# Performance work log

Hardware: AMD Instinct MI355X
Metric: run time of the kernel (lower is better)

## Reference

```python
import jax, jax.numpy as jnp
import numpy as np

N, X_DIM, Y_DIM, HID = 1024, 256, 256, 256  # HID = hidden_size // 2


def setup_inputs() -> dict:
    key = jax.random.key(0)
    ks = jax.random.split(key, 11)
    s_in = 1.0 / np.sqrt(X_DIM)
    s_h = 1.0 / np.sqrt(HID)
    return {
        "x_samples": jax.random.normal(ks[0], (N, X_DIM), jnp.float32),
        "y_samples": jax.random.normal(ks[1], (N, Y_DIM), jnp.float32),
        "z_samples": jax.random.normal(ks[2], (N, Y_DIM), jnp.float32),
        "w1_mu": jax.random.uniform(ks[3], (HID, X_DIM), jnp.float32, -s_in, s_in),
        "b1_mu": jax.random.uniform(ks[4], (HID,), jnp.float32, -s_in, s_in),
        "w2_mu": jax.random.uniform(ks[5], (Y_DIM, HID), jnp.float32, -s_h, s_h),
        "b2_mu": jax.random.uniform(ks[6], (Y_DIM,), jnp.float32, -s_h, s_h),
        "w1_lv": jax.random.uniform(ks[7], (HID, X_DIM), jnp.float32, -s_in, s_in),
        "b1_lv": jax.random.uniform(ks[8], (HID,), jnp.float32, -s_in, s_in),
        "w2_lv": jax.random.uniform(ks[9], (Y_DIM, HID), jnp.float32, -s_h, s_h),
        "b2_lv": jax.random.uniform(ks[10], (Y_DIM,), jnp.float32, -s_h, s_h),
    }


def reference(x_samples, y_samples, z_samples,
              w1_mu, b1_mu, w2_mu, b2_mu,
              w1_lv, b1_lv, w2_lv, b2_lv):
    # MLP heads (torch Linear: x @ W.T + b)
    h_mu = jax.nn.relu(x_samples @ w1_mu.T + b1_mu)
    mu = h_mu @ w2_mu.T + b2_mu                       # [N, D]
    h_lv = jax.nn.relu(x_samples @ w1_lv.T + b1_lv)
    logvar = jnp.tanh(h_lv @ w2_lv.T + b2_lv)          # [N, D]

    inv2var = 1.0 / (2.0 * jnp.exp(logvar))           # [N, D]

    # positive: per-sample conditional log-density term
    positive = -((mu - y_samples) ** 2 + (mu - z_samples) ** 2) * inv2var  # [N, D]

    # negative: mean over all pairings (i: prediction, j: sample)
    # pairwise squared diffs materialize [N, N, D] like the original broadcast
    pred = mu[:, None, :]                              # [N, 1, D]
    sq = (y_samples[None, :, :] - pred) ** 2 + (z_samples[None, :, :] - pred) ** 2
    negative = -sq.mean(axis=1) * inv2var              # [N, D]

    return jax.nn.relu(positive.sum(axis=-1) - negative.sum(axis=-1)).mean()
```

## Files before the change

kernel.cpp:

```cpp
#include <hip/hip_runtime.h>
#include <math.h>

constexpr int LSB = 72;

typedef short bf16x8 __attribute__((ext_vector_type(8)));
typedef float f32x4  __attribute__((ext_vector_type(4)));

__device__ __forceinline__ unsigned short f2bf_rne(float f) {
    unsigned u = __float_as_uint(f);
    unsigned r = (u + 0x7fff + ((u >> 16) & 1)) >> 16;
    return (unsigned short)r;
}
__device__ __forceinline__ float bf2f(unsigned short h) {
    return __uint_as_float(((unsigned)h) << 16);
}
__device__ __forceinline__ void split4(float4 v, ushort4& hi, ushort4& lo) {
    hi.x = f2bf_rne(v.x); lo.x = f2bf_rne(v.x - bf2f(hi.x));
    hi.y = f2bf_rne(v.y); lo.y = f2bf_rne(v.y - bf2f(hi.y));
    hi.z = f2bf_rne(v.z); lo.z = f2bf_rne(v.z - bf2f(hi.z));
    hi.w = f2bf_rne(v.w); lo.w = f2bf_rne(v.w - bf2f(hi.w));
}

__global__ __launch_bounds__(256, 2)
void k1_layer1(const float* __restrict__ x,
               const float* __restrict__ w1m, const float* __restrict__ w1l,
               const float* __restrict__ b1m, const float* __restrict__ b1l,
               const float* __restrict__ w2m, const float* __restrict__ w2l,
               unsigned short* __restrict__ hmH, unsigned short* __restrict__ hmL,
               unsigned short* __restrict__ hlH, unsigned short* __restrict__ hlL,
               unsigned short* __restrict__ w2mH, unsigned short* __restrict__ w2mL,
               unsigned short* __restrict__ w2lH, unsigned short* __restrict__ w2lL,
               const float* __restrict__ y, const float* __restrict__ z,
               float* __restrict__ pA1, float* __restrict__ pB1,
               float* __restrict__ rowAcc) {
    const int bid = blockIdx.x, t = threadIdx.x;

    if (bid >= 512) {
        int m = bid - 512;
        float sA = 0.f, sB = 0.f;
        int base = m * 64 * 256 + t;
        for (int j = 0; j < 64; j++) {
            float yv = y[base + j * 256];
            float zv = z[base + j * 256];
            sA += yv * yv + zv * zv;
            sB += yv + zv;
        }
        pA1[m * 256 + t] = sA;
        pB1[m * 256 + t] = sB;
        return;
    }

    const int head = bid & 1, ct = (bid >> 1) & 7, rt = bid >> 4;
    const int rowBase = rt * 32, colBase = ct * 32;
    const int w = t >> 6, lane = t & 63, quad = lane >> 4, mr = lane & 15;
    const int mt = w & 1, nt = w >> 1;

    const float* Bw   = head ? w1l : w1m;
    const float* bias = head ? b1l : b1m;
    unsigned short* CH = head ? hlH : hmH;
    unsigned short* CL = head ? hlL : hmL;

    __shared__ __align__(16) unsigned short Ah[32][LSB], Al[32][LSB];
    __shared__ __align__(16) unsigned short Bh[32][LSB], Bl[32][LSB];

    f32x4 acc = {0.f, 0.f, 0.f, 0.f};

    for (int kt = 0; kt < 256; kt += 64) {
#pragma unroll
        for (int p = 0; p < 2; p++) {
            int idx = p * 256 + t;
            int r = idx >> 4, k4 = idx & 15;
            float4 av = *(const float4*)&x[(rowBase + r) * 256 + kt + k4 * 4];
            float4 bv = *(const float4*)&Bw[(colBase + r) * 256 + kt + k4 * 4];
            ushort4 h4, l4;
            split4(av, h4, l4);
            *(ushort4*)&Ah[r][k4 * 4] = h4;
            *(ushort4*)&Al[r][k4 * 4] = l4;
            split4(bv, h4, l4);
            *(ushort4*)&Bh[r][k4 * 4] = h4;
            *(ushort4*)&Bl[r][k4 * 4] = l4;
        }
        __syncthreads();

#pragma unroll
        for (int kk = 0; kk < 64; kk += 32) {
            int ko = kk + quad * 8;
            bf16x8 ah = *(const bf16x8*)&Ah[mt * 16 + mr][ko];
            bf16x8 al = *(const bf16x8*)&Al[mt * 16 + mr][ko];
            bf16x8 bh = *(const bf16x8*)&Bh[nt * 16 + mr][ko];
            bf16x8 bl = *(const bf16x8*)&Bl[nt * 16 + mr][ko];
            acc = __builtin_amdgcn_mfma_f32_16x16x32_bf16(ah, bh, acc, 0, 0, 0);
            acc = __builtin_amdgcn_mfma_f32_16x16x32_bf16(ah, bl, acc, 0, 0, 0);
            acc = __builtin_amdgcn_mfma_f32_16x16x32_bf16(al, bh, acc, 0, 0, 0);
        }
        __syncthreads();
    }

    {
        int cg = colBase + nt * 16 + mr;
        float bb = bias[cg];
#pragma unroll
        for (int reg = 0; reg < 4; reg++) {
            int rg = rowBase + mt * 16 + quad * 4 + reg;
            float v = fmaxf(acc[reg] + bb, 0.f);
            unsigned short hi = f2bf_rne(v);
            CH[rg * 256 + cg] = hi;
            CL[rg * 256 + cg] = f2bf_rne(v - bf2f(hi));
        }
    }

    if (bid < 256) {
        int off = bid * 256 + t;
        float vm = w2m[off], vl = w2l[off];
        unsigned short h1 = f2bf_rne(vm);
        w2mH[off] = h1; w2mL[off] = f2bf_rne(vm - bf2f(h1));
        unsigned short h2 = f2bf_rne(vl);
        w2lH[off] = h2; w2lL[off] = f2bf_rne(vl - bf2f(h2));
    }

    if (bid < 4) rowAcc[bid * 256 + t] = 0.f;
}

__global__ __launch_bounds__(256, 2)
void k2_fused(const unsigned short* __restrict__ hmH, const unsigned short* __restrict__ hmL,
              const unsigned short* __restrict__ hlH, const unsigned short* __restrict__ hlL,
              const unsigned short* __restrict__ w2mH, const unsigned short* __restrict__ w2mL,
              const unsigned short* __restrict__ w2lH, const unsigned short* __restrict__ w2lL,
              const float* __restrict__ b2m, const float* __restrict__ b2l,
              const float* __restrict__ y, const float* __restrict__ z,
              const float* __restrict__ pA1, const float* __restrict__ pB1,
              float* __restrict__ rowAcc) {
    const int bid = blockIdx.x, t = threadIdx.x;
    const int rt = bid >> 4, ct = bid & 15;
    const int rowBase = rt * 32, colBase = ct * 16;
    const int w = t >> 6, lane = t & 63, quad = lane >> 4, mr = lane & 15;
    const int h = w & 1, mt = w >> 1;

    __shared__ __align__(16) unsigned short Ast[2][2][32][LSB];
    __shared__ __align__(16) unsigned short Bst[2][2][16][LSB];
    __shared__ float Cx[2][32][17];
    __shared__ float partA[16][16], partB[16][16];
    __shared__ float mAf[16], mBf[16];

    const unsigned short* Aarr[4] = {hmH, hmL, hlH, hlL};
    const unsigned short* Barr[4] = {w2mH, w2mL, w2lH, w2lL};

    {
        int s = t >> 4, c = t & 15;
        partA[s][c] = pA1[s * 256 + colBase + c];
        partB[s][c] = pB1[s * 256 + colBase + c];
    }
    __syncthreads();
    if (t < 16) {
        float sA = 0.f, sB = 0.f;
#pragma unroll
        for (int s = 0; s < 16; s++) { sA += partA[s][t]; sB += partB[s][t]; }
        mAf[t] = sA * (1.f / 1024.f);
        mBf[t] = sB * (1.f / 1024.f);
    }

    f32x4 acc = {0.f, 0.f, 0.f, 0.f};

    for (int kt = 0; kt < 256; kt += 64) {
#pragma unroll
        for (int hp = 0; hp < 4; hp++) {
#pragma unroll
            for (int p = 0; p < 2; p++) {
                int idx = p * 256 + t;
                int r = idx >> 4, k4 = idx & 15;
                *(ushort4*)&Ast[hp >> 1][hp & 1][r][k4 * 4] =
                    *(const ushort4*)&Aarr[hp][(rowBase + r) * 256 + kt + k4 * 4];
            }
            {
                int r = t >> 4, k4 = t & 15;
                *(ushort4*)&Bst[hp >> 1][hp & 1][r][k4 * 4] =
                    *(const ushort4*)&Barr[hp][(colBase + r) * 256 + kt + k4 * 4];
            }
        }
        __syncthreads();

#pragma unroll
        for (int kk = 0; kk < 64; kk += 32) {
            int ko = kk + quad * 8;
            bf16x8 ah = *(const bf16x8*)&Ast[h][0][mt * 16 + mr][ko];
            bf16x8 al = *(const bf16x8*)&Ast[h][1][mt * 16 + mr][ko];
            bf16x8 bh = *(const bf16x8*)&Bst[h][0][mr][ko];
            bf16x8 bl = *(const bf16x8*)&Bst[h][1][mr][ko];
            acc = __builtin_amdgcn_mfma_f32_16x16x32_bf16(ah, bh, acc, 0, 0, 0);
            acc = __builtin_amdgcn_mfma_f32_16x16x32_bf16(ah, bl, acc, 0, 0, 0);
            acc = __builtin_amdgcn_mfma_f32_16x16x32_bf16(al, bh, acc, 0, 0, 0);
        }
        __syncthreads();
    }

    {
        const float* bias = h ? b2l : b2m;
        float bb = bias[colBase + mr];
#pragma unroll
        for (int reg = 0; reg < 4; reg++)
            Cx[h][mt * 16 + quad * 4 + reg][mr] = acc[reg] + bb;
    }
    __syncthreads();

    {
        int col = t & 15, rg = t >> 4;
        int gcol = colBase + col;
        float mA = mAf[col], mB = mBf[col];
#pragma unroll
        for (int rr = 0; rr < 2; rr++) {
            int row = rg * 2 + rr;
            int o = (rowBase + row) * 256 + gcol;
            float m  = Cx[0][row][col];
            float lv = tanhf(Cx[1][row][col]);
            float iv = 0.5f * expf(-lv);
            float yv = y[o];
            float zv = z[o];
            float Mt = mA - 2.f * m * mB + 2.f * m * m;
            float dy = m - yv, dz = m - zv;
            float term = iv * (Mt - dy * dy - dz * dz);
#pragma unroll
            for (int msk = 8; msk; msk >>= 1)
                term += __shfl_xor(term, msk, 16);
            if (col == 0) atomicAdd(&rowAcc[rowBase + row], term);
        }
    }
}

__global__ __launch_bounds__(256)
void k3_final(const float* __restrict__ rowAcc, float* __restrict__ out) {
    __shared__ float red[4];
    int t = threadIdx.x, lane = t & 63, wave = t >> 6;
    float v = 0.f;
#pragma unroll
    for (int p = 0; p < 4; p++)
        v += fmaxf(rowAcc[p * 256 + t], 0.f);
#pragma unroll
    for (int msk = 32; msk; msk >>= 1)
        v += __shfl_xor(v, msk, 64);
    if (lane == 0) red[wave] = v;
    __syncthreads();
    if (t == 0)
        out[0] = (red[0] + red[1] + red[2] + red[3]) * (1.f / 1024.f);
}

extern "C" void kernel_launch(void* const* d_in, const int* in_sizes, int n_in,
                              void* d_out, int out_size, void* d_ws, size_t ws_size,
                              hipStream_t stream) {
    const float* x   = (const float*)d_in[0];
    const float* y   = (const float*)d_in[1];
    const float* zs  = (const float*)d_in[2];
    const float* w1m = (const float*)d_in[3];
    const float* b1m = (const float*)d_in[4];
    const float* w2m = (const float*)d_in[5];
    const float* b2m = (const float*)d_in[6];
    const float* w1l = (const float*)d_in[7];
    const float* b1l = (const float*)d_in[8];
    const float* w2l = (const float*)d_in[9];
    const float* b2l = (const float*)d_in[10];
    float* out = (float*)d_out;

    char* ws = (char*)d_ws;
    float* pA1    = (float*)(ws);
    float* pB1    = (float*)(ws + (256u << 10));
    float* rowAcc = (float*)(ws + (512u << 10));
    unsigned short* hmH = (unsigned short*)(ws + (1024u << 10));
    unsigned short* hmL = (unsigned short*)(ws + (1536u << 10));
    unsigned short* hlH = (unsigned short*)(ws + (2048u << 10));
    unsigned short* hlL = (unsigned short*)(ws + (2560u << 10));
    unsigned short* w2mH = (unsigned short*)(ws + (3072u << 10));
    unsigned short* w2mL = (unsigned short*)(ws + (3200u << 10));
    unsigned short* w2lH = (unsigned short*)(ws + (3328u << 10));
    unsigned short* w2lL = (unsigned short*)(ws + (3456u << 10));

    k1_layer1<<<528, 256, 0, stream>>>(x, w1m, w1l, b1m, b1l, w2m, w2l,
                                       hmH, hmL, hlH, hlL,
                                       w2mH, w2mL, w2lH, w2lL,
                                       y, zs, pA1, pB1, rowAcc);
    k2_fused<<<512, 256, 0, stream>>>(hmH, hmL, hlH, hlL,
                                      w2mH, w2mL, w2lH, w2lL,
                                      b2m, b2l, y, zs, pA1, pB1, rowAcc);
    k3_final<<<1, 256, 0, stream>>>(rowAcc, out);
}
```

Baseline: 92.14 us.

## Fuse both MLP layers and loss into one row-block kernel with double-buffered weights

Splits all weights into bf16 hi/lo in a small prep kernel, which also computes the column sums of y and z and zeroes the output. A single fused kernel then processes 16 rows per block. It keeps the hidden activations in shared memory, streams W1 and W2 tiles through a register-prefetched double buffer, and reduces the loss per row before one atomic per block. This removes the global round trip of the hidden activations and two kernel launches. In exchange it launches only 64 blocks, so most compute units sit idle and each block streams the full weight set serially.

```diff
diff --git a/kernel.cpp b/kernel.cpp
--- a/kernel.cpp
+++ b/kernel.cpp
@@ -21,22 +21,51 @@
     hi.w = f2bf_rne(v.w); lo.w = f2bf_rne(v.w - bf2f(hi.w));
 }
 
-__global__ __launch_bounds__(256, 2)
-void k1_layer1(const float* __restrict__ x,
-               const float* __restrict__ w1m, const float* __restrict__ w1l,
-               const float* __restrict__ b1m, const float* __restrict__ b1l,
-               const float* __restrict__ w2m, const float* __restrict__ w2l,
-               unsigned short* __restrict__ hmH, unsigned short* __restrict__ hmL,
-               unsigned short* __restrict__ hlH, unsigned short* __restrict__ hlL,
-               unsigned short* __restrict__ w2mH, unsigned short* __restrict__ w2mL,
-               unsigned short* __restrict__ w2lH, unsigned short* __restrict__ w2lL,
-               const float* __restrict__ y, const float* __restrict__ z,
-               float* __restrict__ pA1, float* __restrict__ pB1,
-               float* __restrict__ rowAcc) {
+struct Pre { bf16x8 v0, v1, v2, v3; };
+
+__device__ __forceinline__ void stage_load(Pre& p,
+        const unsigned short* __restrict__ H0, const unsigned short* __restrict__ L0,
+        const unsigned short* __restrict__ H1, const unsigned short* __restrict__ L1,
+        int colB, int kB, int t) {
+    int off = (colB + (t >> 3)) * 256 + kB + (t & 7) * 8;
+    p.v0 = *(const bf16x8*)&H0[off];
+    p.v1 = *(const bf16x8*)&L0[off];
+    p.v2 = *(const bf16x8*)&H1[off];
+    p.v3 = *(const bf16x8*)&L1[off];
+}
+__device__ __forceinline__ void stage_write(const Pre& p, unsigned short* b, int t) {
+    unsigned short* d = b + (t >> 3) * LSB + (t & 7) * 8;
+    *(bf16x8*)(d        ) = p.v0;
+    *(bf16x8*)(d +  4608) = p.v1;
+    *(bf16x8*)(d +  9216) = p.v2;
+    *(bf16x8*)(d + 13824) = p.v3;
+}
+
+__global__ __launch_bounds__(256)
+void k0_prep(const float* __restrict__ w1m, const float* __restrict__ w1l,
+             const float* __restrict__ w2m, const float* __restrict__ w2l,
+             const float* __restrict__ y, const float* __restrict__ z,
+             unsigned short* __restrict__ w1mH, unsigned short* __restrict__ w1mL,
+             unsigned short* __restrict__ w1lH, unsigned short* __restrict__ w1lL,
+             unsigned short* __restrict__ w2mH, unsigned short* __restrict__ w2mL,
+             unsigned short* __restrict__ w2lH, unsigned short* __restrict__ w2lL,
+             float* __restrict__ pA1, float* __restrict__ pB1,
+             float* __restrict__ out) {
     const int bid = blockIdx.x, t = threadIdx.x;
-
-    if (bid >= 512) {
-        int m = bid - 512;
+    if (bid < 64) {
+        int off = bid * 1024 + t * 4;
+        float4 v; ushort4 h4, l4;
+        v = *(const float4*)&w1m[off]; split4(v, h4, l4);
+        *(ushort4*)&w1mH[off] = h4; *(ushort4*)&w1mL[off] = l4;
+        v = *(const float4*)&w1l[off]; split4(v, h4, l4);
+        *(ushort4*)&w1lH[off] = h4; *(ushort4*)&w1lL[off] = l4;
+        v = *(const float4*)&w2m[off]; split4(v, h4, l4);
+        *(ushort4*)&w2mH[off] = h4; *(ushort4*)&w2mL[off] = l4;
+        v = *(const float4*)&w2l[off]; split4(v, h4, l4);
+        *(ushort4*)&w2lH[off] = h4; *(ushort4*)&w2lL[off] = l4;
+    } else {
+        int m = bid - 64;
+        if (m == 0 && t == 0) out[0] = 0.f;
         float sA = 0.f, sB = 0.f;
         int base = m * 64 * 256 + t;
         for (int j = 0; j < 64; j++) {
@@ -47,200 +76,152 @@
         }
         pA1[m * 256 + t] = sA;
         pB1[m * 256 + t] = sB;
-        return;
-    }
-
-    const int head = bid & 1, ct = (bid >> 1) & 7, rt = bid >> 4;
-    const int rowBase = rt * 32, colBase = ct * 32;
-    const int w = t >> 6, lane = t & 63, quad = lane >> 4, mr = lane & 15;
-    const int mt = w & 1, nt = w >> 1;
-
-    const float* Bw   = head ? w1l : w1m;
-    const float* bias = head ? b1l : b1m;
-    unsigned short* CH = head ? hlH : hmH;
-    unsigned short* CL = head ? hlL : hmL;
-
-    __shared__ __align__(16) unsigned short Ah[32][LSB], Al[32][LSB];
-    __shared__ __align__(16) unsigned short Bh[32][LSB], Bl[32][LSB];
-
-    f32x4 acc = {0.f, 0.f, 0.f, 0.f};
-
-    for (int kt = 0; kt < 256; kt += 64) {
-#pragma unroll
-        for (int p = 0; p < 2; p++) {
-            int idx = p * 256 + t;
-            int r = idx >> 4, k4 = idx & 15;
-            float4 av = *(const float4*)&x[(rowBase + r) * 256 + kt + k4 * 4];
-            float4 bv = *(const float4*)&Bw[(colBase + r) * 256 + kt + k4 * 4];
-            ushort4 h4, l4;
-            split4(av, h4, l4);
-            *(ushort4*)&Ah[r][k4 * 4] = h4;
-            *(ushort4*)&Al[r][k4 * 4] = l4;
-            split4(bv, h4, l4);
-            *(ushort4*)&Bh[r][k4 * 4] = h4;
-            *(ushort4*)&Bl[r][k4 * 4] = l4;
-        }
-        __syncthreads();
-
-#pragma unroll
-        for (int kk = 0; kk < 64; kk += 32) {
-            int ko = kk + quad * 8;
-            bf16x8 ah = *(const bf16x8*)&Ah[mt * 16 + mr][ko];
-            bf16x8 al = *(const bf16x8*)&Al[mt * 16 + mr][ko];
-            bf16x8 bh = *(const bf16x8*)&Bh[nt * 16 + mr][ko];
-            bf16x8 bl = *(const bf16x8*)&Bl[nt * 16 + mr][ko];
-            acc = __builtin_amdgcn_mfma_f32_16x16x32_bf16(ah, bh, acc, 0, 0, 0);
-            acc = __builtin_amdgcn_mfma_f32_16x16x32_bf16(ah, bl, acc, 0, 0, 0);
-            acc = __builtin_amdgcn_mfma_f32_16x16x32_bf16(al, bh, acc, 0, 0, 0);
-        }
-        __syncthreads();
-    }
-
-    {
-        int cg = colBase + nt * 16 + mr;
-        float bb = bias[cg];
+    }
+}
+
+__global__ __launch_bounds__(512)
+void kf_fused(const float* __restrict__ x, const float* __restrict__ y, const float* __restrict__ z,
+              const float* __restrict__ b1m, const float* __restrict__ b1l,
+              const float* __restrict__ b2m, const float* __restrict__ b2l,
+              const unsigned short* __restrict__ w1mH, const unsigned short* __restrict__ w1mL,
+              const unsigned short* __restrict__ w1lH, const unsigned short* __restrict__ w1lL,
+              const unsigned short* __restrict__ w2mH, const unsigned short* __restrict__ w2mL,
+              const unsigned short* __restrict__ w2lH, const unsigned short* __restrict__ w2lL,
+              const float* __restrict__ pA1, const float* __restrict__ pB1,
+              float* __restrict__ out) {
+    const int bid = blockIdx.x, t = threadIdx.x;
+    const int R0 = bid << 4;
+    const int lane = t & 63, quad = lane >> 4, mr = lane & 15;
+    const int wv = t >> 6, h = wv & 1, nt = wv >> 1;
+
+    __shared__ __align__(16) unsigned short Ax[2][16][264];
+    __shared__ __align__(16) unsigned short Hb[2][2][16][264];
+    __shared__ __align__(16) unsigned short BtF[2][18432];
+    __shared__ float Cx[2][16][68];
+    __shared__ float mAf[256], mBf[256], rowSum[16];
+
+    if (t < 256) {
+        float sA = 0.f, sB = 0.f;
+#pragma unroll
+        for (int sI = 0; sI < 16; sI++) { sA += pA1[sI * 256 + t]; sB += pB1[sI * 256 + t]; }
+        mAf[t] = sA * (1.f / 1024.f);
+        mBf[t] = sB * (1.f / 1024.f);
+    }
+    if (t < 16) rowSum[t] = 0.f;
+#pragma unroll
+    for (int p = 0; p < 2; p++) {
+        int idx = p * 512 + t;
+        int r = idx >> 6, k4 = idx & 63;
+        float4 av = *(const float4*)&x[(R0 + r) * 256 + k4 * 4];
+        ushort4 h4, l4; split4(av, h4, l4);
+        *(ushort4*)&Ax[0][r][k4 * 4] = h4;
+        *(ushort4*)&Ax[1][r][k4 * 4] = l4;
+    }
+
+    Pre pre;
+    stage_load(pre, w1mH, w1mL, w1lH, w1lL, 0, 0, t);
+
+    int s = 0;
+    for (int cg = 0; cg < 4; cg++) {
+        f32x4 acc = {0.f, 0.f, 0.f, 0.f};
+        for (int kt = 0; kt < 4; kt++, s++) {
+            unsigned short* b = BtF[s & 1];
+            stage_write(pre, b, t);
+            if (s < 15) stage_load(pre, w1mH, w1mL, w1lH, w1lL,
+                                   ((s + 1) >> 2) << 6, ((s + 1) & 3) << 6, t);
+            else        stage_load(pre, w2mH, w2mL, w2lH, w2lL, 0, 0, t);
+            __syncthreads();
+            const unsigned short* bHp = b + (h * 2 + 0) * 4608 + (nt * 16 + mr) * LSB;
+            const unsigned short* bLp = b + (h * 2 + 1) * 4608 + (nt * 16 + mr) * LSB;
+            const unsigned short* aHp = &Ax[0][mr][kt * 64];
+            const unsigned short* aLp = &Ax[1][mr][kt * 64];
+#pragma unroll
+            for (int ks = 0; ks < 2; ks++) {
+                int ko = ks * 32 + quad * 8;
+                bf16x8 ah = *(const bf16x8*)&aHp[ko];
+                bf16x8 al = *(const bf16x8*)&aLp[ko];
+                bf16x8 bh = *(const bf16x8*)&bHp[ko];
+                bf16x8 bl = *(const bf16x8*)&bLp[ko];
+                acc = __builtin_amdgcn_mfma_f32_16x16x32_bf16(ah, bh, acc, 0, 0, 0);
+                acc = __builtin_amdgcn_mfma_f32_16x16x32_bf16(ah, bl, acc, 0, 0, 0);
+                acc = __builtin_amdgcn_mfma_f32_16x16x32_bf16(al, bh, acc, 0, 0, 0);
+            }
+        }
+        int gcol = cg * 64 + nt * 16 + mr;
+        float bb = (h ? b1l : b1m)[gcol];
 #pragma unroll
         for (int reg = 0; reg < 4; reg++) {
-            int rg = rowBase + mt * 16 + quad * 4 + reg;
             float v = fmaxf(acc[reg] + bb, 0.f);
             unsigned short hi = f2bf_rne(v);
-            CH[rg * 256 + cg] = hi;
-            CL[rg * 256 + cg] = f2bf_rne(v - bf2f(hi));
-        }
-    }
-
-    if (bid < 256) {
-        int off = bid * 256 + t;
-        float vm = w2m[off], vl = w2l[off];
-        unsigned short h1 = f2bf_rne(vm);
-        w2mH[off] = h1; w2mL[off] = f2bf_rne(vm - bf2f(h1));
-        unsigned short h2 = f2bf_rne(vl);
-        w2lH[off] = h2; w2lL[off] = f2bf_rne(vl - bf2f(h2));
-    }
-
-    if (bid < 4) rowAcc[bid * 256 + t] = 0.f;
-}
-
-__global__ __launch_bounds__(256, 2)
-void k2_fused(const unsigned short* __restrict__ hmH, const unsigned short* __restrict__ hmL,
-              const unsigned short* __restrict__ hlH, const unsigned short* __restrict__ hlL,
-              const unsigned short* __restrict__ w2mH, const unsigned short* __restrict__ w2mL,
-              const unsigned short* __restrict__ w2lH, const unsigned short* __restrict__ w2lL,
-              const float* __restrict__ b2m, const float* __restrict__ b2l,
-              const float* __restrict__ y, const float* __restrict__ z,
-              const float* __restrict__ pA1, const float* __restrict__ pB1,
-              float* __restrict__ rowAcc) {
-    const int bid = blockIdx.x, t = threadIdx.x;
-    const int rt = bid >> 4, ct = bid & 15;
-    const int rowBase = rt * 32, colBase = ct * 16;
-    const int w = t >> 6, lane = t & 63, quad = lane >> 4, mr = lane & 15;
-    const int h = w & 1, mt = w >> 1;
-
-    __shared__ __align__(16) unsigned short Ast[2][2][32][LSB];
-    __shared__ __align__(16) unsigned short Bst[2][2][16][LSB];
-    __shared__ float Cx[2][32][17];
-    __shared__ float partA[16][16], partB[16][16];
-    __shared__ float mAf[16], mBf[16];
-
-    const unsigned short* Aarr[4] = {hmH, hmL, hlH, hlL};
-    const unsigned short* Barr[4] = {w2mH, w2mL, w2lH, w2lL};
-
-    {
-        int s = t >> 4, c = t & 15;
-        partA[s][c] = pA1[s * 256 + colBase + c];
-        partB[s][c] = pB1[s * 256 + colBase + c];
-    }
-    __syncthreads();
+            Hb[h][0][quad * 4 + reg][gcol] = hi;
+            Hb[h][1][quad * 4 + reg][gcol] = f2bf_rne(v - bf2f(hi));
+        }
+    }
+
+    for (int cg = 0; cg < 4; cg++) {
+        f32x4 acc = {0.f, 0.f, 0.f, 0.f};
+        for (int kt = 0; kt < 4; kt++, s++) {
+            unsigned short* b = BtF[s & 1];
+            stage_write(pre, b, t);
+            if (s < 31) {
+                int nn = s - 15;
+                stage_load(pre, w2mH, w2mL, w2lH, w2lL, (nn >> 2) << 6, (nn & 3) << 6, t);
+            }
+            __syncthreads();
+            const unsigned short* bHp = b + (h * 2 + 0) * 4608 + (nt * 16 + mr) * LSB;
+            const unsigned short* bLp = b + (h * 2 + 1) * 4608 + (nt * 16 + mr) * LSB;
+            const unsigned short* aHp = &Hb[h][0][mr][kt * 64];
+            const unsigned short* aLp = &Hb[h][1][mr][kt * 64];
+#pragma unroll
+            for (int ks = 0; ks < 2; ks++) {
+                int ko = ks * 32 + quad * 8;
+                bf16x8 ah = *(const bf16x8*)&aHp[ko];
+                bf16x8 al = *(const bf16x8*)&aLp[ko];
+                bf16x8 bh = *(const bf16x8*)&bHp[ko];
+                bf16x8 bl = *(const bf16x8*)&bLp[ko];
+                acc = __builtin_amdgcn_mfma_f32_16x16x32_bf16(ah, bh, acc, 0, 0, 0);
+                acc = __builtin_amdgcn_mfma_f32_16x16x32_bf16(ah, bl, acc, 0, 0, 0);
+                acc = __builtin_amdgcn_mfma_f32_16x16x32_bf16(al, bh, acc, 0, 0, 0);
+            }
+        }
+        {
+            float bb = (h ? b2l : b2m)[cg * 64 + nt * 16 + mr];
+#pragma unroll
+            for (int reg = 0; reg < 4; reg++)
+                Cx[h][quad * 4 + reg][nt * 16 + mr] = acc[reg] + bb;
+        }
+        __syncthreads();
+        {
+            int r = t >> 5, c0 = t & 31;
+            float v = 0.f;
+#pragma unroll
+            for (int j = 0; j < 2; j++) {
+                int c = c0 + 32 * j;
+                int gcol = cg * 64 + c;
+                float m  = Cx[0][r][c];
+                float lv = tanhf(Cx[1][r][c]);
+                float iv = 0.5f * expf(-lv);
+                int o = (R0 + r) * 256 + gcol;
+                float yv = y[o], zv = z[o];
+                float Mt = mAf[gcol] - 2.f * m * mBf[gcol] + 2.f * m * m;
+                float dy = m - yv, dz = m - zv;
+                v += iv * (Mt - dy * dy - dz * dz);
+            }
+#pragma unroll
+            for (int msk = 16; msk; msk >>= 1)
+                v += __shfl_xor(v, msk, 32);
+            if (c0 == 0) rowSum[r] += v;
+        }
+        __syncthreads();
+    }
+
     if (t < 16) {
-        float sA = 0.f, sB = 0.f;
-#pragma unroll
-        for (int s = 0; s < 16; s++) { sA += partA[s][t]; sB += partB[s][t]; }
-        mAf[t] = sA * (1.f / 1024.f);
-        mBf[t] = sB * (1.f / 1024.f);
-    }
-
-    f32x4 acc = {0.f, 0.f, 0.f, 0.f};
-
-    for (int kt = 0; kt < 256; kt += 64) {
-#pragma unroll
-        for (int hp = 0; hp < 4; hp++) {
-#pragma unroll
-            for (int p = 0; p < 2; p++) {
-                int idx = p * 256 + t;
-                int r = idx >> 4, k4 = idx & 15;
-                *(ushort4*)&Ast[hp >> 1][hp & 1][r][k4 * 4] =
-                    *(const ushort4*)&Aarr[hp][(rowBase + r) * 256 + kt + k4 * 4];
-            }
-            {
-                int r = t >> 4, k4 = t & 15;
-                *(ushort4*)&Bst[hp >> 1][hp & 1][r][k4 * 4] =
-                    *(const ushort4*)&Barr[hp][(colBase + r) * 256 + kt + k4 * 4];
-            }
-        }
-        __syncthreads();
-
-#pragma unroll
-        for (int kk = 0; kk < 64; kk += 32) {
-            int ko = kk + quad * 8;
-            bf16x8 ah = *(const bf16x8*)&Ast[h][0][mt * 16 + mr][ko];
-            bf16x8 al = *(const bf16x8*)&Ast[h][1][mt * 16 + mr][ko];
-            bf16x8 bh = *(const bf16x8*)&Bst[h][0][mr][ko];
-            bf16x8 bl = *(const bf16x8*)&Bst[h][1][mr][ko];
-            acc = __builtin_amdgcn_mfma_f32_16x16x32_bf16(ah, bh, acc, 0, 0, 0);
-            acc = __builtin_amdgcn_mfma_f32_16x16x32_bf16(ah, bl, acc, 0, 0, 0);
-            acc = __builtin_amdgcn_mfma_f32_16x16x32_bf16(al, bh, acc, 0, 0, 0);
-        }
-        __syncthreads();
-    }
-
-    {
-        const float* bias = h ? b2l : b2m;
-        float bb = bias[colBase + mr];
-#pragma unroll
-        for (int reg = 0; reg < 4; reg++)
-            Cx[h][mt * 16 + quad * 4 + reg][mr] = acc[reg] + bb;
-    }
-    __syncthreads();
-
-    {
-        int col = t & 15, rg = t >> 4;
-        int gcol = colBase + col;
-        float mA = mAf[col], mB = mBf[col];
-#pragma unroll
-        for (int rr = 0; rr < 2; rr++) {
-            int row = rg * 2 + rr;
-            int o = (rowBase + row) * 256 + gcol;
-            float m  = Cx[0][row][col];
-            float lv = tanhf(Cx[1][row][col]);
-            float iv = 0.5f * expf(-lv);
-            float yv = y[o];
-            float zv = z[o];
-            float Mt = mA - 2.f * m * mB + 2.f * m * m;
-            float dy = m - yv, dz = m - zv;
-            float term = iv * (Mt - dy * dy - dz * dz);
-#pragma unroll
-            for (int msk = 8; msk; msk >>= 1)
-                term += __shfl_xor(term, msk, 16);
-            if (col == 0) atomicAdd(&rowAcc[rowBase + row], term);
-        }
-    }
-}
-
-__global__ __launch_bounds__(256)
-void k3_final(const float* __restrict__ rowAcc, float* __restrict__ out) {
-    __shared__ float red[4];
-    int t = threadIdx.x, lane = t & 63, wave = t >> 6;
-    float v = 0.f;
-#pragma unroll
-    for (int p = 0; p < 4; p++)
-        v += fmaxf(rowAcc[p * 256 + t], 0.f);
-#pragma unroll
-    for (int msk = 32; msk; msk >>= 1)
-        v += __shfl_xor(v, msk, 64);
-    if (lane == 0) red[wave] = v;
-    __syncthreads();
-    if (t == 0)
-        out[0] = (red[0] + red[1] + red[2] + red[3]) * (1.f / 1024.f);
+        float v = fmaxf(rowSum[t], 0.f);
+#pragma unroll
+        for (int msk = 8; msk; msk >>= 1)
+            v += __shfl_xor(v, msk, 16);
+        if (t == 0) atomicAdd(out, v * (1.f / 1024.f));
+    }
 }
 
 extern "C" void kernel_launch(void* const* d_in, const int* in_sizes, int n_in,
@@ -260,24 +241,23 @@
     float* out = (float*)d_out;
 
     char* ws = (char*)d_ws;
-    float* pA1    = (float*)(ws);
-    float* pB1    = (float*)(ws + (256u << 10));
-    float* rowAcc = (float*)(ws + (512u << 10));
-    unsigned short* hmH = (unsigned short*)(ws + (1024u << 10));
-    unsigned short* hmL = (unsigned short*)(ws + (1536u << 10));
-    unsigned short* hlH = (unsigned short*)(ws + (2048u << 10));
-    unsigned short* hlL = (unsigned short*)(ws + (2560u << 10));
-    unsigned short* w2mH = (unsigned short*)(ws + (3072u << 10));
-    unsigned short* w2mL = (unsigned short*)(ws + (3200u << 10));
-    unsigned short* w2lH = (unsigned short*)(ws + (3328u << 10));
-    unsigned short* w2lL = (unsigned short*)(ws + (3456u << 10));
-
-    k1_layer1<<<528, 256, 0, stream>>>(x, w1m, w1l, b1m, b1l, w2m, w2l,
-                                       hmH, hmL, hlH, hlL,
-                                       w2mH, w2mL, w2lH, w2lL,
-                                       y, zs, pA1, pB1, rowAcc);
-    k2_fused<<<512, 256, 0, stream>>>(hmH, hmL, hlH, hlL,
-                                      w2mH, w2mL, w2lH, w2lL,
-                                      b2m, b2l, y, zs, pA1, pB1, rowAcc);
-    k3_final<<<1, 256, 0, stream>>>(rowAcc, out);
-}
+    float* pA1 = (float*)(ws);
+    float* pB1 = (float*)(ws + (64u  << 10));
+    unsigned short* w1mH = (unsigned short*)(ws + (128u  << 10));
+    unsigned short* w1mL = (unsigned short*)(ws + (256u  << 10));
+    unsigned short* w1lH = (unsigned short*)(ws + (384u  << 10));
+    unsigned short* w1lL = (unsigned short*)(ws + (512u  << 10));
+    unsigned short* w2mH = (unsigned short*)(ws + (640u  << 10));
+    unsigned short* w2mL = (unsigned short*)(ws + (768u  << 10));
+    unsigned short* w2lH = (unsigned short*)(ws + (896u  << 10));
+    unsigned short* w2lL = (unsigned short*)(ws + (1024u << 10));
+
+    k0_prep<<<80, 256, 0, stream>>>(w1m, w1l, w2m, w2l, y, zs,
+                                    w1mH, w1mL, w1lH, w1lL,
+                                    w2mH, w2mL, w2lH, w2lL,
+                                    pA1, pB1, out);
+    kf_fused<<<64, 512, 0, stream>>>(x, y, zs, b1m, b1l, b2m, b2l,
+                                     w1mH, w1mL, w1lH, w1lL,
+                                     w2mH, w2mL, w2lH, w2lL,
+                                     pA1, pB1, out);
+}
```

Result: slower. 98.24 us (+6.6%).

## Load MFMA operands directly from global memory, dropping LDS staging in both GEMMs

Applied to the files above, without the earlier changes.

Both GEMM kernels stop staging tiles in shared memory with __syncthreads and instead have each lane load its MFMA fragments (8 contiguous elements per k-step) straight from global memory. The first kernel converts fp32 to hi/lo bf16 in registers per fragment. This removes LDS traffic and barriers. The cost is redundant global/L2 reads: operands shared across waves are now fetched separately by each wave, and the hi/lo split in the first kernel is recomputed per wave instead of once per tile.

```diff
diff --git a/kernel.cpp b/kernel.cpp
--- a/kernel.cpp
+++ b/kernel.cpp
@@ -1,7 +1,6 @@
 #include <hip/hip_runtime.h>
 #include <math.h>
 
-constexpr int LSB = 72;
 
 typedef short bf16x8 __attribute__((ext_vector_type(8)));
 typedef float f32x4  __attribute__((ext_vector_type(4)));
@@ -19,6 +18,18 @@
     hi.y = f2bf_rne(v.y); lo.y = f2bf_rne(v.y - bf2f(hi.y));
     hi.z = f2bf_rne(v.z); lo.z = f2bf_rne(v.z - bf2f(hi.z));
     hi.w = f2bf_rne(v.w); lo.w = f2bf_rne(v.w - bf2f(hi.w));
+}
+__device__ __forceinline__ void split8(const float* __restrict__ p,
+                                       bf16x8& hi, bf16x8& lo) {
+    float4 v0 = *(const float4*)p;
+    float4 v1 = *(const float4*)(p + 4);
+    float a[8] = {v0.x, v0.y, v0.z, v0.w, v1.x, v1.y, v1.z, v1.w};
+#pragma unroll
+    for (int i = 0; i < 8; i++) {
+        unsigned short h = f2bf_rne(a[i]);
+        hi[i] = (short)h;
+        lo[i] = (short)f2bf_rne(a[i] - bf2f(h));
+    }
 }
 
 __global__ __launch_bounds__(256, 2)
@@ -60,40 +71,19 @@
     unsigned short* CH = head ? hlH : hmH;
     unsigned short* CL = head ? hlL : hmL;
 
-    __shared__ __align__(16) unsigned short Ah[32][LSB], Al[32][LSB];
-    __shared__ __align__(16) unsigned short Bh[32][LSB], Bl[32][LSB];
+    const float* ax = &x [(rowBase + mt * 16 + mr) * 256];
+    const float* bw = &Bw[(colBase + nt * 16 + mr) * 256];
 
     f32x4 acc = {0.f, 0.f, 0.f, 0.f};
-
-    for (int kt = 0; kt < 256; kt += 64) {
-#pragma unroll
-        for (int p = 0; p < 2; p++) {
-            int idx = p * 256 + t;
-            int r = idx >> 4, k4 = idx & 15;
-            float4 av = *(const float4*)&x[(rowBase + r) * 256 + kt + k4 * 4];
-            float4 bv = *(const float4*)&Bw[(colBase + r) * 256 + kt + k4 * 4];
-            ushort4 h4, l4;
-            split4(av, h4, l4);
-            *(ushort4*)&Ah[r][k4 * 4] = h4;
-            *(ushort4*)&Al[r][k4 * 4] = l4;
-            split4(bv, h4, l4);
-            *(ushort4*)&Bh[r][k4 * 4] = h4;
-            *(ushort4*)&Bl[r][k4 * 4] = l4;
-        }
-        __syncthreads();
-
-#pragma unroll
-        for (int kk = 0; kk < 64; kk += 32) {
-            int ko = kk + quad * 8;
-            bf16x8 ah = *(const bf16x8*)&Ah[mt * 16 + mr][ko];
-            bf16x8 al = *(const bf16x8*)&Al[mt * 16 + mr][ko];
-            bf16x8 bh = *(const bf16x8*)&Bh[nt * 16 + mr][ko];
-            bf16x8 bl = *(const bf16x8*)&Bl[nt * 16 + mr][ko];
-            acc = __builtin_amdgcn_mfma_f32_16x16x32_bf16(ah, bh, acc, 0, 0, 0);
-            acc = __builtin_amdgcn_mfma_f32_16x16x32_bf16(ah, bl, acc, 0, 0, 0);
-            acc = __builtin_amdgcn_mfma_f32_16x16x32_bf16(al, bh, acc, 0, 0, 0);
-        }
-        __syncthreads();
+#pragma unroll
+    for (int ks = 0; ks < 8; ks++) {
+        int k0 = ks * 32 + quad * 8;
+        bf16x8 ah, al, bh, bl;
+        split8(&ax[k0], ah, al);
+        split8(&bw[k0], bh, bl);
+        acc = __builtin_amdgcn_mfma_f32_16x16x32_bf16(ah, bh, acc, 0, 0, 0);
+        acc = __builtin_amdgcn_mfma_f32_16x16x32_bf16(ah, bl, acc, 0, 0, 0);
+        acc = __builtin_amdgcn_mfma_f32_16x16x32_bf16(al, bh, acc, 0, 0, 0);
     }
 
     {
@@ -136,15 +126,10 @@
     const int w = t >> 6, lane = t & 63, quad = lane >> 4, mr = lane & 15;
     const int h = w & 1, mt = w >> 1;
 
-    __shared__ __align__(16) unsigned short Ast[2][2][32][LSB];
-    __shared__ __align__(16) unsigned short Bst[2][2][16][LSB];
     __shared__ float Cx[2][32][17];
     __shared__ float partA[16][16], partB[16][16];
     __shared__ float mAf[16], mBf[16];
 
-    const unsigned short* Aarr[4] = {hmH, hmL, hlH, hlL};
-    const unsigned short* Barr[4] = {w2mH, w2mL, w2lH, w2lL};
-
     {
         int s = t >> 4, c = t & 15;
         partA[s][c] = pA1[s * 256 + colBase + c];
@@ -159,38 +144,26 @@
         mBf[t] = sB * (1.f / 1024.f);
     }
 
+    const unsigned short* AH = h ? hlH : hmH;
+    const unsigned short* AL = h ? hlL : hmL;
+    const unsigned short* BH = h ? w2lH : w2mH;
+    const unsigned short* BL = h ? w2lL : w2mL;
+    const unsigned short* aH = &AH[(rowBase + mt * 16 + mr) * 256];
+    const unsigned short* aL = &AL[(rowBase + mt * 16 + mr) * 256];
+    const unsigned short* bH = &BH[(colBase + mr) * 256];
+    const unsigned short* bL = &BL[(colBase + mr) * 256];
+
     f32x4 acc = {0.f, 0.f, 0.f, 0.f};
-
-    for (int kt = 0; kt < 256; kt += 64) {
-#pragma unroll
-        for (int hp = 0; hp < 4; hp++) {
-#pragma unroll
-            for (int p = 0; p < 2; p++) {
-                int idx = p * 256 + t;
-                int r = idx >> 4, k4 = idx & 15;
-                *(ushort4*)&Ast[hp >> 1][hp & 1][r][k4 * 4] =
-                    *(const ushort4*)&Aarr[hp][(rowBase + r) * 256 + kt + k4 * 4];
-            }
-            {
-                int r = t >> 4, k4 = t & 15;
-                *(ushort4*)&Bst[hp >> 1][hp & 1][r][k4 * 4] =
-                    *(const ushort4*)&Barr[hp][(colBase + r) * 256 + kt + k4 * 4];
-            }
-        }
-        __syncthreads();
-
-#pragma unroll
-        for (int kk = 0; kk < 64; kk += 32) {
-            int ko = kk + quad * 8;
-            bf16x8 ah = *(const bf16x8*)&Ast[h][0][mt * 16 + mr][ko];
-            bf16x8 al = *(const bf16x8*)&Ast[h][1][mt * 16 + mr][ko];
-            bf16x8 bh = *(const bf16x8*)&Bst[h][0][mr][ko];
-            bf16x8 bl = *(const bf16x8*)&Bst[h][1][mr][ko];
-            acc = __builtin_amdgcn_mfma_f32_16x16x32_bf16(ah, bh, acc, 0, 0, 0);
-            acc = __builtin_amdgcn_mfma_f32_16x16x32_bf16(ah, bl, acc, 0, 0, 0);
-            acc = __builtin_amdgcn_mfma_f32_16x16x32_bf16(al, bh, acc, 0, 0, 0);
-        }
-        __syncthreads();
+#pragma unroll
+    for (int ks = 0; ks < 8; ks++) {
+        int k0 = ks * 32 + quad * 8;
+        bf16x8 ah = *(const bf16x8*)&aH[k0];
+        bf16x8 al = *(const bf16x8*)&aL[k0];
+        bf16x8 bh = *(const bf16x8*)&bH[k0];
+        bf16x8 bl = *(const bf16x8*)&bL[k0];
+        acc = __builtin_amdgcn_mfma_f32_16x16x32_bf16(ah, bh, acc, 0, 0, 0);
+        acc = __builtin_amdgcn_mfma_f32_16x16x32_bf16(ah, bl, acc, 0, 0, 0);
+        acc = __builtin_amdgcn_mfma_f32_16x16x32_bf16(al, bh, acc, 0, 0, 0);
     }
 
     {
```

Result: slower. 96.98 us (+5.3%).

## Load full-K layer1 tiles once and fold y/z column sums into GEMM blocks

Applied to the files above, without the earlier changes.

Layer-1 GEMM blocks now stage the whole K=256 slice of x and W1 (hi/lo bf16 split) into LDS in one pass, then run all MFMA steps without the per-64-K reload and barrier pairs. The separate 16 reduction blocks for y/z column statistics are removed, and the first 64 GEMM blocks compute 16-row partial sums instead. k2 now sums 64 partials per column instead of 16. The larger LDS footprint (about 67KB per block) may lower occupancy and drops the overlap of loads with MFMA.

```diff
diff --git a/kernel.cpp b/kernel.cpp
--- a/kernel.cpp
+++ b/kernel.cpp
@@ -1,7 +1,7 @@
 #include <hip/hip_runtime.h>
 #include <math.h>
 
-constexpr int LSB = 72;
+constexpr int LSK = 264;
 
 typedef short bf16x8 __attribute__((ext_vector_type(8)));
 typedef float f32x4  __attribute__((ext_vector_type(4)));
@@ -35,21 +35,6 @@
                float* __restrict__ rowAcc) {
     const int bid = blockIdx.x, t = threadIdx.x;
 
-    if (bid >= 512) {
-        int m = bid - 512;
-        float sA = 0.f, sB = 0.f;
-        int base = m * 64 * 256 + t;
-        for (int j = 0; j < 64; j++) {
-            float yv = y[base + j * 256];
-            float zv = z[base + j * 256];
-            sA += yv * yv + zv * zv;
-            sB += yv + zv;
-        }
-        pA1[m * 256 + t] = sA;
-        pB1[m * 256 + t] = sB;
-        return;
-    }
-
     const int head = bid & 1, ct = (bid >> 1) & 7, rt = bid >> 4;
     const int rowBase = rt * 32, colBase = ct * 32;
     const int w = t >> 6, lane = t & 63, quad = lane >> 4, mr = lane & 15;
@@ -60,40 +45,41 @@
     unsigned short* CH = head ? hlH : hmH;
     unsigned short* CL = head ? hlL : hmL;
 
-    __shared__ __align__(16) unsigned short Ah[32][LSB], Al[32][LSB];
-    __shared__ __align__(16) unsigned short Bh[32][LSB], Bl[32][LSB];
+    __shared__ __align__(16) unsigned short Ah[32][LSK], Al[32][LSK];
+    __shared__ __align__(16) unsigned short Bh[32][LSK], Bl[32][LSK];
+
+#pragma unroll
+    for (int p = 0; p < 8; p++) {
+        int idx = p * 256 + t;
+        int r = idx >> 6, k4 = idx & 63;
+        float4 av = *(const float4*)&x [(rowBase + r) * 256 + k4 * 4];
+        float4 bv = *(const float4*)&Bw[(colBase + r) * 256 + k4 * 4];
+        ushort4 h4, l4;
+        split4(av, h4, l4);
+        *(ushort4*)&Ah[r][k4 * 4] = h4;
+        *(ushort4*)&Al[r][k4 * 4] = l4;
+        split4(bv, h4, l4);
+        *(ushort4*)&Bh[r][k4 * 4] = h4;
+        *(ushort4*)&Bl[r][k4 * 4] = l4;
+    }
+    __syncthreads();
+
+    const unsigned short* aHp = &Ah[mt * 16 + mr][0];
+    const unsigned short* aLp = &Al[mt * 16 + mr][0];
+    const unsigned short* bHp = &Bh[nt * 16 + mr][0];
+    const unsigned short* bLp = &Bl[nt * 16 + mr][0];
 
     f32x4 acc = {0.f, 0.f, 0.f, 0.f};
-
-    for (int kt = 0; kt < 256; kt += 64) {
-#pragma unroll
-        for (int p = 0; p < 2; p++) {
-            int idx = p * 256 + t;
-            int r = idx >> 4, k4 = idx & 15;
-            float4 av = *(const float4*)&x[(rowBase + r) * 256 + kt + k4 * 4];
-            float4 bv = *(const float4*)&Bw[(colBase + r) * 256 + kt + k4 * 4];
-            ushort4 h4, l4;
-            split4(av, h4, l4);
-            *(ushort4*)&Ah[r][k4 * 4] = h4;
-            *(ushort4*)&Al[r][k4 * 4] = l4;
-            split4(bv, h4, l4);
-            *(ushort4*)&Bh[r][k4 * 4] = h4;
-            *(ushort4*)&Bl[r][k4 * 4] = l4;
-        }
-        __syncthreads();
-
-#pragma unroll
-        for (int kk = 0; kk < 64; kk += 32) {
-            int ko = kk + quad * 8;
-            bf16x8 ah = *(const bf16x8*)&Ah[mt * 16 + mr][ko];
-            bf16x8 al = *(const bf16x8*)&Al[mt * 16 + mr][ko];
-            bf16x8 bh = *(const bf16x8*)&Bh[nt * 16 + mr][ko];
-            bf16x8 bl = *(const bf16x8*)&Bl[nt * 16 + mr][ko];
-            acc = __builtin_amdgcn_mfma_f32_16x16x32_bf16(ah, bh, acc, 0, 0, 0);
-            acc = __builtin_amdgcn_mfma_f32_16x16x32_bf16(ah, bl, acc, 0, 0, 0);
-            acc = __builtin_amdgcn_mfma_f32_16x16x32_bf16(al, bh, acc, 0, 0, 0);
-        }
-        __syncthreads();
+#pragma unroll
+    for (int ks = 0; ks < 8; ks++) {
+        int ko = ks * 32 + quad * 8;
+        bf16x8 ah = *(const bf16x8*)&aHp[ko];
+        bf16x8 al = *(const bf16x8*)&aLp[ko];
+        bf16x8 bh = *(const bf16x8*)&bHp[ko];
+        bf16x8 bl = *(const bf16x8*)&bLp[ko];
+        acc = __builtin_amdgcn_mfma_f32_16x16x32_bf16(ah, bh, acc, 0, 0, 0);
+        acc = __builtin_amdgcn_mfma_f32_16x16x32_bf16(ah, bl, acc, 0, 0, 0);
+        acc = __builtin_amdgcn_mfma_f32_16x16x32_bf16(al, bh, acc, 0, 0, 0);
     }
 
     {
@@ -118,8 +104,24 @@
         w2lH[off] = h2; w2lL[off] = f2bf_rne(vl - bf2f(h2));
     }
 
+    if (bid < 64) {
+        float sA = 0.f, sB = 0.f;
+        int base = bid * 16 * 256 + t;
+#pragma unroll 4
+        for (int j = 0; j < 16; j++) {
+            float yv = y[base + j * 256];
+            float zv = z[base + j * 256];
+            sA += yv * yv + zv * zv;
+            sB += yv + zv;
+        }
+        pA1[bid * 256 + t] = sA;
+        pB1[bid * 256 + t] = sB;
+    }
+
     if (bid < 4) rowAcc[bid * 256 + t] = 0.f;
 }
+
+constexpr int LSB = 72;
 
 __global__ __launch_bounds__(256, 2)
 void k2_fused(const unsigned short* __restrict__ hmH, const unsigned short* __restrict__ hmL,
@@ -147,8 +149,14 @@
 
     {
         int s = t >> 4, c = t & 15;
-        partA[s][c] = pA1[s * 256 + colBase + c];
-        partB[s][c] = pB1[s * 256 + colBase + c];
+        float a0 = 0.f, b0 = 0.f;
+#pragma unroll
+        for (int j = 0; j < 4; j++) {
+            a0 += pA1[(s * 4 + j) * 256 + colBase + c];
+            b0 += pB1[(s * 4 + j) * 256 + colBase + c];
+        }
+        partA[s][c] = a0;
+        partB[s][c] = b0;
     }
     __syncthreads();
     if (t < 16) {
@@ -272,7 +280,7 @@
     unsigned short* w2lH = (unsigned short*)(ws + (3328u << 10));
     unsigned short* w2lL = (unsigned short*)(ws + (3456u << 10));
 
-    k1_layer1<<<528, 256, 0, stream>>>(x, w1m, w1l, b1m, b1l, w2m, w2l,
+    k1_layer1<<<512, 256, 0, stream>>>(x, w1m, w1l, b1m, b1l, w2m, w2l,
                                        hmH, hmL, hlH, hlL,
                                        w2mH, w2mL, w2lH, w2lL,
                                        y, zs, pA1, pB1, rowAcc);
```

Measured after the change: 91.44 us. About the same (-0.8%).
